# Performance work log

Measured on AMD Instinct MI355X. Metric: run time of the kernel, lower is better.

## Reference

```python
import jax, jax.numpy as jnp
import numpy as np

N = 100000      # nodes
E = 1250000     # edges
D = 64          # d_data
H = 256         # hidden dim
C = 40          # n_cls
K = 4           # propagation steps
ALPHA = 0.05
EPS = 1e-5      # BatchNorm eps


def setup_inputs() -> dict:
    key = jax.random.key(0)
    ks = jax.random.split(key, 8)
    feat = jax.random.normal(ks[0], (N, D), dtype=jnp.float32)
    src = jax.random.randint(ks[1], (E,), 0, N, dtype=jnp.int32)
    dst = jax.random.randint(ks[2], (E,), 0, N, dtype=jnp.int32)
    W1 = jax.random.normal(ks[3], (D, H), dtype=jnp.float32) * (1.0 / np.sqrt(D))
    W2 = jax.random.normal(ks[4], (H, H), dtype=jnp.float32) * (1.0 / np.sqrt(H))
    W3 = jax.random.normal(ks[5], (H, C), dtype=jnp.float32) * (1.0 / np.sqrt(H))
    return {
        "feat": feat, "src": src, "dst": dst,
        "W1": W1, "b1": jnp.zeros((H,), jnp.float32),
        "g1": jnp.ones((H,), jnp.float32), "be1": jnp.zeros((H,), jnp.float32),
        "W2": W2, "b2": jnp.zeros((H,), jnp.float32),
        "g2": jnp.ones((H,), jnp.float32), "be2": jnp.zeros((H,), jnp.float32),
        "W3": W3, "b3": jnp.zeros((C,), jnp.float32),
    }


def _batchnorm(x, gamma, beta):
    # BatchNorm1d in training mode: per-feature batch mean / biased var
    mu = jnp.mean(x, axis=0)
    var = jnp.var(x, axis=0)
    return gamma * (x - mu) * jax.lax.rsqrt(var + EPS) + beta


def reference(feat, src, dst, W1, b1, g1, be1, W2, b2, g2, be2, W3, b3):
    # --- S2GC aggregation: sum_{t=1..K} (D^-1/2 A D^-1/2)^t X ---
    deg = jax.ops.segment_sum(jnp.ones((E,), feat.dtype), dst, num_segments=N)
    norm = jnp.clip(deg, 1.0, None) ** -0.5          # [N]
    norm = norm[:, None]                              # [N,1]
    h = feat
    acc = jnp.zeros_like(feat)
    for _ in range(K):
        h = h * norm
        h = jax.ops.segment_sum(h[src], dst, num_segments=N)  # copy_u -> sum
        h = h * norm
        acc = acc + h
    x = (1.0 - ALPHA) / K * acc + ALPHA * feat
    # --- feat_trans MLP: (Linear -> BN -> ReLU) x2 -> Linear ---
    x = jax.nn.relu(_batchnorm(x @ W1 + b1, g1, be1))
    x = jax.nn.relu(_batchnorm(x @ W2 + b2, g2, be2))
    logits = x @ W3 + b3                              # mask is all-ones (tasks=None)
    return logits
```

## Files before the change

### kernel.cpp

```cpp
#include <hip/hip_runtime.h>

#define NN 100000
#define EE 1250000
#define DD 64
#define HH 256
#define NC_OUT 40
#define ALPHA_C 0.05f
#define COEF 0.2375f
#define EPS_C 1e-5f
#define NBUCK 391
#define EPB 8192
#define GB1 1563
#define NRED 16

typedef __attribute__((ext_vector_type(8))) short short8;
typedef __attribute__((ext_vector_type(4))) float f32x4;

static __device__ __forceinline__ float bf2f(unsigned int u) {
  union { float f; unsigned int i; } x; x.i = u << 16; return x.f;
}
static __device__ __forceinline__ unsigned short f2bf(float f) {
  unsigned int x = __float_as_uint(f);
  unsigned int r = (x + 0x7FFFu + ((x >> 16) & 1u)) >> 16;
  return (unsigned short)r;
}


__global__ void k_count(const int* __restrict__ dst, int* __restrict__ deg) {
  int e = blockIdx.x * 256 + threadIdx.x;
  if (e < EE) atomicAdd(&deg[dst[e]], 1);
}

__global__ void k_scan1(const int* __restrict__ deg, int* __restrict__ rp,
                        int* __restrict__ bsum) {
  __shared__ int ts[256];
  int t = threadIdx.x;
  int base = blockIdx.x * 2048 + t * 8;
  int v[8]; int s = 0;
#pragma unroll
  for (int l = 0; l < 8; l++) { int i = base + l; v[l] = (i < NN) ? deg[i] : 0; s += v[l]; }
  ts[t] = s; __syncthreads();
  for (int off = 1; off < 256; off <<= 1) {
    int x = (t >= off) ? ts[t - off] : 0;
    __syncthreads();
    ts[t] += x;
    __syncthreads();
  }
  int run = ts[t] - s;
#pragma unroll
  for (int l = 0; l < 8; l++) { int i = base + l; if (i < NN) rp[i] = run; run += v[l]; }
  if (t == 255) bsum[blockIdx.x] = ts[255];
}

__global__ void k_scan2(const int* __restrict__ bsum, int* __restrict__ boff, int nb) {
  __shared__ int ts[64];
  int t = threadIdx.x;
  int x = (t < nb) ? bsum[t] : 0;
  ts[t] = x; __syncthreads();
  for (int off = 1; off < 64; off <<= 1) {
    int y = (t >= off) ? ts[t - off] : 0;
    __syncthreads();
    ts[t] += y;
    __syncthreads();
  }
  boff[t] = ts[t] - x;
}

__global__ void k_scan3(int* __restrict__ rp, const int* __restrict__ boff,
                        const int* __restrict__ deg, float* __restrict__ norm,
                        int* __restrict__ bcur) {
  int i = blockIdx.x * 256 + threadIdx.x;
  if (i < NN) {
    int r = rp[i] + boff[i >> 11];
    rp[i] = r;
    if ((i & 255) == 0) bcur[i >> 8] = r;
    int d = deg[i]; if (d < 1) d = 1;
    norm[i] = rsqrtf((float)d);
    if (i == 0) rp[NN] = EE;
  }
}

__global__ __launch_bounds__(256) void k_bucket(const int* __restrict__ src,
                                                const int* __restrict__ dst,
                                                int* __restrict__ bcur,
                                                unsigned int* __restrict__ pairbuf) {
  __shared__ int hist[NBUCK];
  __shared__ int gbase[NBUCK];
  __shared__ int lcur[NBUCK];
  int tid = threadIdx.x;
  int e0 = blockIdx.x * EPB;
  int e1 = e0 + EPB; if (e1 > EE) e1 = EE;
  for (int i = tid; i < NBUCK; i += 256) { hist[i] = 0; lcur[i] = 0; }
  __syncthreads();
  for (int e = e0 + tid; e < e1; e += 256) {
    int b = dst[e] >> 8;
    atomicAdd(&hist[b], 1);
  }
  __syncthreads();
  for (int b = tid; b < NBUCK; b += 256) {
    int h = hist[b];
    gbase[b] = h ? atomicAdd(&bcur[b], h) : 0;
  }
  __syncthreads();
  for (int e = e0 + tid; e < e1; e += 256) {
    int d = dst[e];
    int b = d >> 8;
    int r = atomicAdd(&lcur[b], 1);
    pairbuf[gbase[b] + r] = (unsigned int)src[e] | ((unsigned int)(d & 255) << 24);
  }
}

__global__ __launch_bounds__(256) void k_local(const unsigned int* __restrict__ pairbuf,
                                               const int* __restrict__ rp,
                                               int* __restrict__ srt) {
  __shared__ int cur[256];
  int b = blockIdx.x;
  int node0 = b << 8;
  int t = threadIdx.x;
  int node = node0 + t;
  cur[t] = (node < NN) ? rp[node] : 0;
  int lo = rp[node0];
  int hi = (node0 + 256 <= NN) ? rp[node0 + 256] : EE;
  __syncthreads();
  for (int e = lo + t; e < hi; e += 256) {
    unsigned int w = pairbuf[e];
    int s = (int)(w & 0x1FFFFu);
    int l = (int)(w >> 24);
    int p = atomicAdd(&cur[l], 1);
    srt[p] = s;
  }
}


__global__ void k_init(const float4* __restrict__ feat4, const float* __restrict__ norm,
                       uint2* __restrict__ hs, float4* __restrict__ acc4) {
  int i = blockIdx.x * 256 + threadIdx.x;
  if (i < NN * 16) {
    float nv = norm[i >> 4];
    float4 f = feat4[i];
    uint2 o;
    o.x = (unsigned int)f2bf(f.x * nv) | ((unsigned int)f2bf(f.y * nv) << 16);
    o.y = (unsigned int)f2bf(f.z * nv) | ((unsigned int)f2bf(f.w * nv) << 16);
    hs[i] = o;
    acc4[i] = make_float4(0.f, 0.f, 0.f, 0.f);
  }
}

__global__ void k_gather(const unsigned short* __restrict__ hin,
                         unsigned short* __restrict__ hout,
                         float* __restrict__ accum, const int* __restrict__ rp,
                         const int* __restrict__ srt, const float* __restrict__ norm) {
  int node = blockIdx.x * 4 + (threadIdx.x >> 6);
  int lane = threadIdx.x & 63;
  if (node >= NN) return;
  int beg = rp[node], end = rp[node + 1];
  float s0 = 0.f, s1 = 0.f;
  int e = beg;
  for (; e + 8 <= end; e += 8) {
    int n0 = srt[e], n1 = srt[e + 1], n2 = srt[e + 2], n3 = srt[e + 3];
    int n4 = srt[e + 4], n5 = srt[e + 5], n6 = srt[e + 6], n7 = srt[e + 7];
    float x0 = bf2f(hin[(size_t)n0 * 64 + lane]);
    float x1 = bf2f(hin[(size_t)n1 * 64 + lane]);
    float x2 = bf2f(hin[(size_t)n2 * 64 + lane]);
    float x3 = bf2f(hin[(size_t)n3 * 64 + lane]);
    float x4 = bf2f(hin[(size_t)n4 * 64 + lane]);
    float x5 = bf2f(hin[(size_t)n5 * 64 + lane]);
    float x6 = bf2f(hin[(size_t)n6 * 64 + lane]);
    float x7 = bf2f(hin[(size_t)n7 * 64 + lane]);
    s0 += (x0 + x1) + (x2 + x3);
    s1 += (x4 + x5) + (x6 + x7);
  }
  if (e + 4 <= end) {
    int n0 = srt[e], n1 = srt[e + 1], n2 = srt[e + 2], n3 = srt[e + 3];
    float x0 = bf2f(hin[(size_t)n0 * 64 + lane]);
    float x1 = bf2f(hin[(size_t)n1 * 64 + lane]);
    float x2 = bf2f(hin[(size_t)n2 * 64 + lane]);
    float x3 = bf2f(hin[(size_t)n3 * 64 + lane]);
    s0 += (x0 + x1);
    s1 += (x2 + x3);
    e += 4;
  }
  if (e + 2 <= end) {
    int n0 = srt[e], n1 = srt[e + 1];
    s0 += bf2f(hin[(size_t)n0 * 64 + lane]);
    s1 += bf2f(hin[(size_t)n1 * 64 + lane]);
    e += 2;
  }
  if (e < end) s0 += bf2f(hin[(size_t)srt[e] * 64 + lane]);
  float nv = norm[node];
  float h = (s0 + s1) * nv;
  size_t o = (size_t)node * 64 + lane;
  accum[o] += h;
  hout[o] = f2bf(h * nv);
}

__global__ void k_transW(const float* __restrict__ W, unsigned short* __restrict__ WT, int K) {
  int c = blockIdx.x;
  for (int k = threadIdx.x; k < K; k += blockDim.x)
    WT[(size_t)c * K + k] = f2bf(W[(size_t)k * 256 + c]);
}

template <int KTOT, int MODE>
__global__ __launch_bounds__(256) void k_mfma(
    const void* __restrict__ A0, const float* __restrict__ A1,
    const float* __restrict__ af, const float* __restrict__ cf,
    const unsigned short* __restrict__ BT,
    unsigned short* __restrict__ Yout,
    float* __restrict__ part, int M) {
  constexpr int LDA = 40;
  __shared__ unsigned short Al[64 * LDA];
  __shared__ float afl[256], cfl[256];
  const int tid = threadIdx.x;
  const int wid = tid >> 6, lane = tid & 63;
  const int rbase = blockIdx.x * 64;
  const int nbase = wid * 64;
  const int lr = lane & 15;
  const int kg = lane >> 4;

  if constexpr (MODE == 1) {
    afl[tid] = af[tid];
    cfl[tid] = cf[tid];
    __syncthreads();
  }

  f32x4 acc[4][4];
#pragma unroll
  for (int i = 0; i < 4; i++)
#pragma unroll
    for (int j = 0; j < 4; j++) acc[i][j] = (f32x4){0.f, 0.f, 0.f, 0.f};

  for (int k0 = 0; k0 < KTOT; k0 += 32) {
    {
      int r = tid >> 2;
      int c8 = (tid & 3) * 8;
      int row = rbase + r; if (row >= M) row = M - 1;
      float xv[8];
      if constexpr (MODE == 0) {
        const float* ap = (const float*)A0 + (size_t)row * 64 + k0 + c8;
        const float* fp = A1 + (size_t)row * 64 + k0 + c8;
        float4 a0 = *(const float4*)ap, a1v = *(const float4*)(ap + 4);
        float4 f0 = *(const float4*)fp, f1 = *(const float4*)(fp + 4);
        xv[0] = COEF * a0.x + ALPHA_C * f0.x; xv[1] = COEF * a0.y + ALPHA_C * f0.y;
        xv[2] = COEF * a0.z + ALPHA_C * f0.z; xv[3] = COEF * a0.w + ALPHA_C * f0.w;
        xv[4] = COEF * a1v.x + ALPHA_C * f1.x; xv[5] = COEF * a1v.y + ALPHA_C * f1.y;
        xv[6] = COEF * a1v.z + ALPHA_C * f1.z; xv[7] = COEF * a1v.w + ALPHA_C * f1.w;
      } else {
        const unsigned short* Yp = (const unsigned short*)A0 + (size_t)row * 256 + k0 + c8;
        uint4 v = *(const uint4*)Yp;
        unsigned int u[4] = { v.x, v.y, v.z, v.w };
#pragma unroll
        for (int h = 0; h < 4; h++) {
          int kc = k0 + c8 + h * 2;
          xv[h * 2]     = fmaxf(fmaf(afl[kc],     bf2f(u[h] & 0xffffu), cfl[kc]),     0.f);
          xv[h * 2 + 1] = fmaxf(fmaf(afl[kc + 1], bf2f(u[h] >> 16),     cfl[kc + 1]), 0.f);
        }
      }
      uint4 pk;
      pk.x = (unsigned int)f2bf(xv[0]) | ((unsigned int)f2bf(xv[1]) << 16);
      pk.y = (unsigned int)f2bf(xv[2]) | ((unsigned int)f2bf(xv[3]) << 16);
      pk.z = (unsigned int)f2bf(xv[4]) | ((unsigned int)f2bf(xv[5]) << 16);
      pk.w = (unsigned int)f2bf(xv[6]) | ((unsigned int)f2bf(xv[7]) << 16);
      *(uint4*)&Al[r * LDA + c8] = pk;
    }
    __syncthreads();

    short8 bfrag[4];
#pragma unroll
    for (int ni = 0; ni < 4; ni++) {
      int col = nbase + ni * 16 + lr;
      bfrag[ni] = *(const short8*)(BT + (size_t)col * KTOT + k0 + kg * 8);
    }
    short8 afrag[4];
#pragma unroll
    for (int mi = 0; mi < 4; mi++) {
      afrag[mi] = *(const short8*)&Al[(mi * 16 + lr) * LDA + kg * 8];
    }
#pragma unroll
    for (int mi = 0; mi < 4; mi++)
#pragma unroll
      for (int ni = 0; ni < 4; ni++)
        acc[mi][ni] = __builtin_amdgcn_mfma_f32_16x16x32_bf16(afrag[mi], bfrag[ni],
                                                              acc[mi][ni], 0, 0, 0);
    __syncthreads();
  }

#pragma unroll
  for (int mi = 0; mi < 4; mi++) {
#pragma unroll
    for (int reg = 0; reg < 4; reg++) {
      int row = rbase + mi * 16 + kg * 4 + reg;
      if (row < M) {
#pragma unroll
        for (int ni = 0; ni < 4; ni++) {
          int col = nbase + ni * 16 + lr;
          Yout[(size_t)row * 256 + col] = f2bf(acc[mi][ni][reg]);
        }
      }
    }
  }

  float s4[4] = {0.f, 0.f, 0.f, 0.f};
  float q4[4] = {0.f, 0.f, 0.f, 0.f};
#pragma unroll
  for (int mi = 0; mi < 4; mi++) {
#pragma unroll
    for (int reg = 0; reg < 4; reg++) {
      int row = rbase + mi * 16 + kg * 4 + reg;
      if (row < M) {
#pragma unroll
        for (int ni = 0; ni < 4; ni++) {
          float v = acc[mi][ni][reg];
          s4[ni] += v;
          q4[ni] = fmaf(v, v, q4[ni]);
        }
      }
    }
  }
  float* pb = part + (size_t)blockIdx.x * 512;
#pragma unroll
  for (int ni = 0; ni < 4; ni++) {
    float s = s4[ni], q = q4[ni];
    s += __shfl_xor(s, 16); s += __shfl_xor(s, 32);
    q += __shfl_xor(q, 16); q += __shfl_xor(q, 32);
    if (kg == 0) {
      int col = nbase + ni * 16 + lr;
      pb[col] = s;
      pb[256 + col] = q;
    }
  }
}

__global__ __launch_bounds__(512) void k_red(const float* __restrict__ part,
                                             float* __restrict__ red2) {
  int t = threadIdx.x;
  const int per = (GB1 + NRED - 1) / NRED;
  int b0 = blockIdx.x * per;
  int b1 = b0 + per; if (b1 > GB1) b1 = GB1;
  float s = 0.f;
  for (int b = b0; b < b1; b++) s += part[(size_t)b * 512 + t];
  red2[(size_t)blockIdx.x * 512 + t] = s;
}

__global__ void k_fold(const float* __restrict__ red2,
                       const float* __restrict__ gam, const float* __restrict__ bet,
                       float* __restrict__ af, float* __restrict__ cfv) {
  int c = threadIdx.x;
  float s = 0.f, q = 0.f;
#pragma unroll
  for (int r = 0; r < NRED; r++) {
    s += red2[(size_t)r * 512 + c];
    q += red2[(size_t)r * 512 + 256 + c];
  }
  float m = s * (1.0f / NN);
  float var = q * (1.0f / NN) - m * m;
  float a = gam[c] * rsqrtf(var + EPS_C);
  af[c] = a;
  cfv[c] = bet[c] - m * a;
}

__global__ __launch_bounds__(256) void k_gemm3(
    const unsigned short* __restrict__ Y2, const float* __restrict__ af,
    const float* __restrict__ cfv, const float* __restrict__ W3,
    const float* __restrict__ b3, float* __restrict__ out, int M) {
  __shared__ float Al[256 * 33];
  __shared__ float Wl[256 * 40];
  __shared__ float afl[256], cfl[256];
  int tid = threadIdx.x;
#pragma unroll
  for (int l = 0; l < 40; l++) Wl[l * 256 + tid] = W3[l * 256 + tid];
  afl[tid] = af[tid]; cfl[tid] = cfv[tid];
  __syncthreads();
  int rbase = blockIdx.x * 256;
  int rg = tid >> 3;
  int cg = tid & 7;
  float acc[8][5];
#pragma unroll
  for (int i = 0; i < 8; i++)
#pragma unroll
    for (int j = 0; j < 5; j++) acc[i][j] = 0.f;

  for (int k0 = 0; k0 < 256; k0 += 32) {
    int row = rbase + tid; if (row >= M) row = M - 1;
    const uint4* p = (const uint4*)(Y2 + (size_t)row * 256 + k0);
    uint4 vv[4]; vv[0] = p[0]; vv[1] = p[1]; vv[2] = p[2]; vv[3] = p[3];
    float* ap = &Al[tid * 33];
#pragma unroll
    for (int q = 0; q < 4; q++) {
      unsigned int u[4] = { vv[q].x, vv[q].y, vv[q].z, vv[q].w };
#pragma unroll
      for (int h = 0; h < 4; h++) {
        int kc = k0 + q * 8 + h * 2;
        float x0 = bf2f(u[h] & 0xffffu);
        float x1 = bf2f(u[h] >> 16);
        x0 = fmaxf(fmaf(afl[kc], x0, cfl[kc]), 0.f);
        x1 = fmaxf(fmaf(afl[kc + 1], x1, cfl[kc + 1]), 0.f);
        ap[q * 8 + h * 2] = x0; ap[q * 8 + h * 2 + 1] = x1;
      }
    }
    __syncthreads();
#pragma unroll 4
    for (int kk = 0; kk < 32; kk++) {
      float b[5];
#pragma unroll
      for (int j = 0; j < 5; j++) b[j] = Wl[(k0 + kk) * 40 + cg * 5 + j];
#pragma unroll
      for (int i = 0; i < 8; i++) {
        float a = Al[(rg + 32 * i) * 33 + kk];
#pragma unroll
        for (int j = 0; j < 5; j++) acc[i][j] = fmaf(a, b[j], acc[i][j]);
      }
    }
    __syncthreads();
  }
#pragma unroll
  for (int i = 0; i < 8; i++) {
    int row = rbase + rg + 32 * i;
    if (row < M) {
#pragma unroll
      for (int j = 0; j < 5; j++)
        out[(size_t)row * 40 + cg * 5 + j] = acc[i][j] + b3[cg * 5 + j];
    }
  }
}


extern "C" void kernel_launch(void* const* d_in, const int* in_sizes, int n_in,
                              void* d_out, int out_size, void* d_ws, size_t ws_size,
                              hipStream_t stream) {
  const float* feat = (const float*)d_in[0];
  const int* src = (const int*)d_in[1];
  const int* dstv = (const int*)d_in[2];
  const float* W1 = (const float*)d_in[3];
  const float* g1 = (const float*)d_in[5];
  const float* be1 = (const float*)d_in[6];
  const float* W2 = (const float*)d_in[7];
  const float* g2 = (const float*)d_in[9];
  const float* be2 = (const float*)d_in[10];
  const float* W3 = (const float*)d_in[11];
  const float* b3 = (const float*)d_in[12];
  float* out = (float*)d_out;

  char* w = (char*)d_ws;
  size_t off = 0;
  auto alloc = [&](size_t bytes) -> char* {
    char* p = w + off;
    off = (off + bytes + 255) & ~(size_t)255;
    return p;
  };
  int* deg = (int*)alloc((size_t)NN * 4);
  int* rp = (int*)alloc((size_t)(NN + 1) * 4);
  int* bsum = (int*)alloc(256);
  int* boff = (int*)alloc(256);
  int* bcur = (int*)alloc((size_t)NBUCK * 4);
  float* norm = (float*)alloc((size_t)NN * 4);
  int* srt = (int*)alloc((size_t)EE * 4);
  unsigned int* pairbuf = (unsigned int*)alloc((size_t)EE * 4);
  unsigned short* hsA = (unsigned short*)alloc((size_t)NN * 64 * 2);
  unsigned short* hsB = (unsigned short*)alloc((size_t)NN * 64 * 2);
  float* accb = (float*)alloc((size_t)NN * 64 * 4);
  unsigned short* Y1 = (unsigned short*)alloc((size_t)NN * 256 * 2);
  unsigned short* Y2 = (unsigned short*)alloc((size_t)NN * 256 * 2);
  unsigned short* W1T = (unsigned short*)alloc(256 * 64 * 2);
  unsigned short* W2T = (unsigned short*)alloc(256 * 256 * 2);
  float* part = (float*)alloc((size_t)GB1 * 512 * 4);
  float* red2 = (float*)alloc((size_t)NRED * 512 * 4);
  float* a1 = (float*)alloc(256 * 4);
  float* c1 = (float*)alloc(256 * 4);
  float* a2 = (float*)alloc(256 * 4);
  float* c2 = (float*)alloc(256 * 4);

  hipMemsetAsync(deg, 0, (size_t)NN * 4, stream);

  const int EB = (EE + 255) / 256;
  const int NB = (NN + 255) / 256;
  const int SB = (NN + 2047) / 2048;
  const int BB = (EE + EPB - 1) / EPB;

  k_count<<<EB, 256, 0, stream>>>(dstv, deg);
  k_transW<<<256, 64, 0, stream>>>(W1, W1T, 64);
  k_transW<<<256, 256, 0, stream>>>(W2, W2T, 256);
  k_scan1<<<SB, 256, 0, stream>>>(deg, rp, bsum);
  k_scan2<<<1, 64, 0, stream>>>(bsum, boff, SB);
  k_scan3<<<NB, 256, 0, stream>>>(rp, boff, deg, norm, bcur);
  k_bucket<<<BB, 256, 0, stream>>>(src, dstv, bcur, pairbuf);
  k_local<<<NBUCK, 256, 0, stream>>>(pairbuf, rp, srt);

  k_init<<<(NN * 16 + 255) / 256, 256, 0, stream>>>((const float4*)feat, norm,
                                                    (uint2*)hsA, (float4*)accb);
  k_gather<<<(NN + 3) / 4, 256, 0, stream>>>(hsA, hsB, accb, rp, srt, norm);
  k_gather<<<(NN + 3) / 4, 256, 0, stream>>>(hsB, hsA, accb, rp, srt, norm);
  k_gather<<<(NN + 3) / 4, 256, 0, stream>>>(hsA, hsB, accb, rp, srt, norm);
  k_gather<<<(NN + 3) / 4, 256, 0, stream>>>(hsB, hsA, accb, rp, srt, norm);

  k_mfma<64, 0><<<GB1, 256, 0, stream>>>(accb, feat, nullptr, nullptr, W1T, Y1, part, NN);
  k_red<<<NRED, 512, 0, stream>>>(part, red2);
  k_fold<<<1, 256, 0, stream>>>(red2, g1, be1, a1, c1);
  k_mfma<256, 1><<<GB1, 256, 0, stream>>>(Y1, nullptr, a1, c1, W2T, Y2, part, NN);
  k_red<<<NRED, 512, 0, stream>>>(part, red2);
  k_fold<<<1, 256, 0, stream>>>(red2, g2, be2, a2, c2);
  k_gemm3<<<NB, 256, 0, stream>>>(Y2, a2, c2, W3, b3, out, NN);
}
```

Baseline: 577.7 us.

## Double-buffer MFMA A tiles, stage output via LDS, prefetch gather indices

The GEMM kernel now double-buffers the A tile in shared memory and loads the next K-slices into registers ahead of use, which removes one barrier per K step and overlaps global loads with MFMA. The output tile is packed to bf16 pairs, staged through a swizzled LDS buffer and written back with coalesced 16-byte stores instead of scattered 2-byte stores. The gather kernel software-prefetches the next 8 neighbor indices before issuing the current feature loads. In exchange the kernel uses more shared memory (32 KB) and more registers, which may reduce occupancy.

```diff
diff --git a/kernel.cpp b/kernel.cpp
--- a/kernel.cpp
+++ b/kernel.cpp
@@ -156,19 +156,31 @@
   int beg = rp[node], end = rp[node + 1];
   float s0 = 0.f, s1 = 0.f;
   int e = beg;
-  for (; e + 8 <= end; e += 8) {
-    int n0 = srt[e], n1 = srt[e + 1], n2 = srt[e + 2], n3 = srt[e + 3];
-    int n4 = srt[e + 4], n5 = srt[e + 5], n6 = srt[e + 6], n7 = srt[e + 7];
-    float x0 = bf2f(hin[(size_t)n0 * 64 + lane]);
-    float x1 = bf2f(hin[(size_t)n1 * 64 + lane]);
-    float x2 = bf2f(hin[(size_t)n2 * 64 + lane]);
-    float x3 = bf2f(hin[(size_t)n3 * 64 + lane]);
-    float x4 = bf2f(hin[(size_t)n4 * 64 + lane]);
-    float x5 = bf2f(hin[(size_t)n5 * 64 + lane]);
-    float x6 = bf2f(hin[(size_t)n6 * 64 + lane]);
-    float x7 = bf2f(hin[(size_t)n7 * 64 + lane]);
-    s0 += (x0 + x1) + (x2 + x3);
-    s1 += (x4 + x5) + (x6 + x7);
+  if (e + 8 <= end) {
+    int i0 = srt[e],     i1 = srt[e + 1], i2 = srt[e + 2], i3 = srt[e + 3];
+    int i4 = srt[e + 4], i5 = srt[e + 5], i6 = srt[e + 6], i7 = srt[e + 7];
+    while (true) {
+      int ne = e + 8;
+      bool more = (ne + 8 <= end);
+      int j0, j1, j2, j3, j4, j5, j6, j7;
+      if (more) {
+        j0 = srt[ne];     j1 = srt[ne + 1]; j2 = srt[ne + 2]; j3 = srt[ne + 3];
+        j4 = srt[ne + 4]; j5 = srt[ne + 5]; j6 = srt[ne + 6]; j7 = srt[ne + 7];
+      }
+      float x0 = bf2f(hin[(size_t)i0 * 64 + lane]);
+      float x1 = bf2f(hin[(size_t)i1 * 64 + lane]);
+      float x2 = bf2f(hin[(size_t)i2 * 64 + lane]);
+      float x3 = bf2f(hin[(size_t)i3 * 64 + lane]);
+      float x4 = bf2f(hin[(size_t)i4 * 64 + lane]);
+      float x5 = bf2f(hin[(size_t)i5 * 64 + lane]);
+      float x6 = bf2f(hin[(size_t)i6 * 64 + lane]);
+      float x7 = bf2f(hin[(size_t)i7 * 64 + lane]);
+      s0 += (x0 + x1) + (x2 + x3);
+      s1 += (x4 + x5) + (x6 + x7);
+      e = ne;
+      if (!more) break;
+      i0 = j0; i1 = j1; i2 = j2; i3 = j3; i4 = j4; i5 = j5; i6 = j6; i7 = j7;
+    }
   }
   if (e + 4 <= end) {
     int n0 = srt[e], n1 = srt[e + 1], n2 = srt[e + 2], n3 = srt[e + 3];
@@ -207,15 +219,23 @@
     const unsigned short* __restrict__ BT,
     unsigned short* __restrict__ Yout,
     float* __restrict__ part, int M) {
+  constexpr int S = KTOT / 32;
   constexpr int LDA = 40;
-  __shared__ unsigned short Al[64 * LDA];
+  __shared__ __align__(16) unsigned char smemraw[32768];
+  unsigned short* const Al0 = (unsigned short*)smemraw;
+  unsigned short* const Al1 = (unsigned short*)(smemraw + 5120);
+  unsigned int* const Cl = (unsigned int*)smemraw;
   __shared__ float afl[256], cfl[256];
+
   const int tid = threadIdx.x;
   const int wid = tid >> 6, lane = tid & 63;
   const int rbase = blockIdx.x * 64;
   const int nbase = wid * 64;
   const int lr = lane & 15;
   const int kg = lane >> 4;
+  const int r = tid >> 2;
+  const int c8 = (tid & 3) * 8;
+  int arow = rbase + r; if (arow >= M) arow = M - 1;
 
   if constexpr (MODE == 1) {
     afl[tid] = af[tid];
@@ -223,81 +243,86 @@
     __syncthreads();
   }
 
+  uint4 rw[2];
+
+  auto LOADX = [&](int s, int buf) {
+    float xv[8];
+    if constexpr (MODE == 0) {
+      const float* ap = (const float*)A0 + (size_t)arow * 64 + s * 32 + c8;
+      const float* fp = A1 + (size_t)arow * 64 + s * 32 + c8;
+      float4 a0 = *(const float4*)ap, a1v = *(const float4*)(ap + 4);
+      float4 f0 = *(const float4*)fp, f1 = *(const float4*)(fp + 4);
+      xv[0] = COEF * a0.x + ALPHA_C * f0.x;  xv[1] = COEF * a0.y + ALPHA_C * f0.y;
+      xv[2] = COEF * a0.z + ALPHA_C * f0.z;  xv[3] = COEF * a0.w + ALPHA_C * f0.w;
+      xv[4] = COEF * a1v.x + ALPHA_C * f1.x; xv[5] = COEF * a1v.y + ALPHA_C * f1.y;
+      xv[6] = COEF * a1v.z + ALPHA_C * f1.z; xv[7] = COEF * a1v.w + ALPHA_C * f1.w;
+    } else {
+      uint4 v = *(const uint4*)((const unsigned short*)A0 + (size_t)arow * 256 + s * 32 + c8);
+      unsigned int u[4] = { v.x, v.y, v.z, v.w };
+#pragma unroll
+      for (int h = 0; h < 4; h++) {
+        int kc = s * 32 + c8 + h * 2;
+        xv[h * 2]     = fmaxf(fmaf(afl[kc],     bf2f(u[h] & 0xffffu), cfl[kc]),     0.f);
+        xv[h * 2 + 1] = fmaxf(fmaf(afl[kc + 1], bf2f(u[h] >> 16),     cfl[kc + 1]), 0.f);
+      }
+    }
+    uint4 pk;
+    pk.x = (unsigned int)f2bf(xv[0]) | ((unsigned int)f2bf(xv[1]) << 16);
+    pk.y = (unsigned int)f2bf(xv[2]) | ((unsigned int)f2bf(xv[3]) << 16);
+    pk.z = (unsigned int)f2bf(xv[4]) | ((unsigned int)f2bf(xv[5]) << 16);
+    pk.w = (unsigned int)f2bf(xv[6]) | ((unsigned int)f2bf(xv[7]) << 16);
+    rw[buf] = pk;
+  };
+
   f32x4 acc[4][4];
 #pragma unroll
   for (int i = 0; i < 4; i++)
 #pragma unroll
     for (int j = 0; j < 4; j++) acc[i][j] = (f32x4){0.f, 0.f, 0.f, 0.f};
 
-  for (int k0 = 0; k0 < KTOT; k0 += 32) {
-    {
-      int r = tid >> 2;
-      int c8 = (tid & 3) * 8;
-      int row = rbase + r; if (row >= M) row = M - 1;
-      float xv[8];
-      if constexpr (MODE == 0) {
-        const float* ap = (const float*)A0 + (size_t)row * 64 + k0 + c8;
-        const float* fp = A1 + (size_t)row * 64 + k0 + c8;
-        float4 a0 = *(const float4*)ap, a1v = *(const float4*)(ap + 4);
-        float4 f0 = *(const float4*)fp, f1 = *(const float4*)(fp + 4);
-        xv[0] = COEF * a0.x + ALPHA_C * f0.x; xv[1] = COEF * a0.y + ALPHA_C * f0.y;
-        xv[2] = COEF * a0.z + ALPHA_C * f0.z; xv[3] = COEF * a0.w + ALPHA_C * f0.w;
-        xv[4] = COEF * a1v.x + ALPHA_C * f1.x; xv[5] = COEF * a1v.y + ALPHA_C * f1.y;
-        xv[6] = COEF * a1v.z + ALPHA_C * f1.z; xv[7] = COEF * a1v.w + ALPHA_C * f1.w;
-      } else {
-        const unsigned short* Yp = (const unsigned short*)A0 + (size_t)row * 256 + k0 + c8;
-        uint4 v = *(const uint4*)Yp;
-        unsigned int u[4] = { v.x, v.y, v.z, v.w };
-#pragma unroll
-        for (int h = 0; h < 4; h++) {
-          int kc = k0 + c8 + h * 2;
-          xv[h * 2]     = fmaxf(fmaf(afl[kc],     bf2f(u[h] & 0xffffu), cfl[kc]),     0.f);
-          xv[h * 2 + 1] = fmaxf(fmaf(afl[kc + 1], bf2f(u[h] >> 16),     cfl[kc + 1]), 0.f);
-        }
-      }
-      uint4 pk;
-      pk.x = (unsigned int)f2bf(xv[0]) | ((unsigned int)f2bf(xv[1]) << 16);
-      pk.y = (unsigned int)f2bf(xv[2]) | ((unsigned int)f2bf(xv[3]) << 16);
-      pk.z = (unsigned int)f2bf(xv[4]) | ((unsigned int)f2bf(xv[5]) << 16);
-      pk.w = (unsigned int)f2bf(xv[6]) | ((unsigned int)f2bf(xv[7]) << 16);
-      *(uint4*)&Al[r * LDA + c8] = pk;
-    }
-    __syncthreads();
-
+  LOADX(0, 0);
+  if constexpr (S > 1) LOADX(1, 1);
+  *(uint4*)&Al0[r * LDA + c8] = rw[0];
+
+#pragma unroll
+  for (int s = 0; s < S; s++) {
+    __syncthreads();
+    const unsigned short* Alr = (s & 1) ? Al1 : Al0;
+    unsigned short* Alw = (s & 1) ? Al0 : Al1;
     short8 bfrag[4];
 #pragma unroll
-    for (int ni = 0; ni < 4; ni++) {
-      int col = nbase + ni * 16 + lr;
-      bfrag[ni] = *(const short8*)(BT + (size_t)col * KTOT + k0 + kg * 8);
-    }
+    for (int ni = 0; ni < 4; ni++)
+      bfrag[ni] = *(const short8*)(BT + (size_t)(nbase + ni * 16 + lr) * KTOT + s * 32 + kg * 8);
+    if (s + 1 < S) *(uint4*)&Alw[r * LDA + c8] = rw[(s + 1) & 1];
+    if (s + 2 < S) LOADX(s + 2, s & 1);
     short8 afrag[4];
 #pragma unroll
-    for (int mi = 0; mi < 4; mi++) {
-      afrag[mi] = *(const short8*)&Al[(mi * 16 + lr) * LDA + kg * 8];
-    }
+    for (int mi = 0; mi < 4; mi++)
+      afrag[mi] = *(const short8*)&Alr[(mi * 16 + lr) * LDA + kg * 8];
 #pragma unroll
     for (int mi = 0; mi < 4; mi++)
 #pragma unroll
       for (int ni = 0; ni < 4; ni++)
         acc[mi][ni] = __builtin_amdgcn_mfma_f32_16x16x32_bf16(afrag[mi], bfrag[ni],
                                                               acc[mi][ni], 0, 0, 0);
-    __syncthreads();
-  }
-
-#pragma unroll
-  for (int mi = 0; mi < 4; mi++) {
-#pragma unroll
-    for (int reg = 0; reg < 4; reg++) {
-      int row = rbase + mi * 16 + kg * 4 + reg;
-      if (row < M) {
-#pragma unroll
-        for (int ni = 0; ni < 4; ni++) {
-          int col = nbase + ni * 16 + lr;
-          Yout[(size_t)row * 256 + col] = f2bf(acc[mi][ni][reg]);
+  }
+
+  __syncthreads();
+#pragma unroll
+  for (int mi = 0; mi < 4; mi++)
+#pragma unroll
+    for (int ni = 0; ni < 4; ni++)
+#pragma unroll
+      for (int reg = 0; reg < 4; reg++) {
+        float v = acc[mi][ni][reg];
+        float pv = __shfl_xor(v, 1);
+        if (!(lr & 1)) {
+          int row = mi * 16 + kg * 4 + reg;
+          int cd = (nbase >> 1) + ni * 8 + (lr >> 1);
+          unsigned int pk = (unsigned int)f2bf(v) | ((unsigned int)f2bf(pv) << 16);
+          Cl[row * 128 + (cd ^ (kg << 3))] = pk;
         }
       }
-    }
-  }
 
   float s4[4] = {0.f, 0.f, 0.f, 0.f};
   float q4[4] = {0.f, 0.f, 0.f, 0.f};
@@ -327,6 +352,19 @@
       pb[col] = s;
       pb[256 + col] = q;
     }
+  }
+
+  __syncthreads();
+#pragma unroll
+  for (int p = 0; p < 8; p++) {
+    int flat = p * 256 + tid;
+    int row = flat >> 5;
+    int u4 = flat & 31;
+    int m = ((row >> 2) & 3) << 3;
+    uint4 vv = *(const uint4*)&Cl[row * 128 + ((u4 * 4) ^ m)];
+    int grow = rbase + row;
+    if (grow < M)
+      *(uint4*)(Yout + (size_t)grow * 256 + u4 * 8) = vv;
   }
 }
 
```

New measurement: 603.7 us. 4.5% more time.

## Drop fp32 accumulator; keep per-step bf16 hops and sum them in GEMM1

Applied to the files above, without the earlier changes.

The gather kernels no longer read-modify-write a float32 accumulator each step. Each propagation step now writes its own bf16 buffer holding h*norm^2, and the first MFMA GEMM sums the four buffers and rescales by sqrt(deg)*COEF while loading the A tile. This removes about 25 MB of fp32 accumulator traffic per step and the zeroing in k_init, at the cost of extra buffers and bf16 rounding on every stored hop. Separately, the MFMA kernels move to 512-thread blocks with 128-row tiles, and weights are pre-laid out per 32-wide K slice so B fragment loads are contiguous.

```diff
diff --git a/kernel.cpp b/kernel.cpp
--- a/kernel.cpp
+++ b/kernel.cpp
@@ -10,7 +10,8 @@
 #define EPS_C 1e-5f
 #define NBUCK 391
 #define EPB 8192
-#define GB1 1563
+#define NB2 782
+#define PART_ROWS (NB2 * 2)
 #define NRED 16
 
 typedef __attribute__((ext_vector_type(8))) short short8;
@@ -23,6 +24,10 @@
   unsigned int x = __float_as_uint(f);
   unsigned int r = (x + 0x7FFFu + ((x >> 16) & 1u)) >> 16;
   return (unsigned short)r;
+}
+static __device__ __forceinline__ float bfat(uint4 v, int j) {
+  unsigned int u = ((const unsigned int*)&v)[j >> 1];
+  return bf2f((j & 1) ? (u >> 16) : (u & 0xffffu));
 }
 
 
@@ -68,7 +73,7 @@
 
 __global__ void k_scan3(int* __restrict__ rp, const int* __restrict__ boff,
                         const int* __restrict__ deg, float* __restrict__ norm,
-                        int* __restrict__ bcur) {
+                        float* __restrict__ rnorm, int* __restrict__ bcur) {
   int i = blockIdx.x * 256 + threadIdx.x;
   if (i < NN) {
     int r = rp[i] + boff[i >> 11];
@@ -76,6 +81,7 @@
     if ((i & 255) == 0) bcur[i >> 8] = r;
     int d = deg[i]; if (d < 1) d = 1;
     norm[i] = rsqrtf((float)d);
+    rnorm[i] = sqrtf((float)d);
     if (i == 0) rp[NN] = EE;
   }
 }
@@ -133,7 +139,7 @@
 
 
 __global__ void k_init(const float4* __restrict__ feat4, const float* __restrict__ norm,
-                       uint2* __restrict__ hs, float4* __restrict__ acc4) {
+                       uint2* __restrict__ hs) {
   int i = blockIdx.x * 256 + threadIdx.x;
   if (i < NN * 16) {
     float nv = norm[i >> 4];
@@ -142,13 +148,12 @@
     o.x = (unsigned int)f2bf(f.x * nv) | ((unsigned int)f2bf(f.y * nv) << 16);
     o.y = (unsigned int)f2bf(f.z * nv) | ((unsigned int)f2bf(f.w * nv) << 16);
     hs[i] = o;
-    acc4[i] = make_float4(0.f, 0.f, 0.f, 0.f);
   }
 }
 
 __global__ void k_gather(const unsigned short* __restrict__ hin,
                          unsigned short* __restrict__ hout,
-                         float* __restrict__ accum, const int* __restrict__ rp,
+                         const int* __restrict__ rp,
                          const int* __restrict__ srt, const float* __restrict__ norm) {
   int node = blockIdx.x * 4 + (threadIdx.x >> 6);
   int lane = threadIdx.x & 63;
@@ -188,38 +193,46 @@
   }
   if (e < end) s0 += bf2f(hin[(size_t)srt[e] * 64 + lane]);
   float nv = norm[node];
-  float h = (s0 + s1) * nv;
-  size_t o = (size_t)node * 64 + lane;
-  accum[o] += h;
-  hout[o] = f2bf(h * nv);
-}
-
-__global__ void k_transW(const float* __restrict__ W, unsigned short* __restrict__ WT, int K) {
-  int c = blockIdx.x;
-  for (int k = threadIdx.x; k < K; k += blockDim.x)
-    WT[(size_t)c * K + k] = f2bf(W[(size_t)k * 256 + c]);
+  hout[(size_t)node * 64 + lane] = f2bf((s0 + s1) * nv * nv);
+}
+
+__global__ void k_transWT(const float* __restrict__ W, unsigned short* __restrict__ BTt,
+                          int K) {
+  int col = blockIdx.x;
+  int t = threadIdx.x;
+  if (t >= (K >> 3)) return;
+  int s = t >> 2, kg = t & 3;
+  size_t o = (size_t)s * 8192 + (size_t)col * 32 + kg * 8;
+#pragma unroll
+  for (int j = 0; j < 8; j++)
+    BTt[o + j] = f2bf(W[(size_t)(s * 32 + kg * 8 + j) * 256 + col]);
 }
 
 template <int KTOT, int MODE>
-__global__ __launch_bounds__(256) void k_mfma(
-    const void* __restrict__ A0, const float* __restrict__ A1,
+__global__ __launch_bounds__(512) void k_mfma(
+    const unsigned short* __restrict__ h1, const unsigned short* __restrict__ h2,
+    const unsigned short* __restrict__ h3, const unsigned short* __restrict__ h4,
+    const float* __restrict__ feat, const float* __restrict__ rnorm,
+    const unsigned short* __restrict__ Yin,
     const float* __restrict__ af, const float* __restrict__ cf,
-    const unsigned short* __restrict__ BT,
-    unsigned short* __restrict__ Yout,
-    float* __restrict__ part, int M) {
+    const unsigned short* __restrict__ BTt,
+    unsigned short* __restrict__ Yout, float* __restrict__ part, int M) {
+  constexpr int S = KTOT / 32;
   constexpr int LDA = 40;
-  __shared__ unsigned short Al[64 * LDA];
+  __shared__ unsigned short Al[128 * LDA];
   __shared__ float afl[256], cfl[256];
   const int tid = threadIdx.x;
   const int wid = tid >> 6, lane = tid & 63;
-  const int rbase = blockIdx.x * 64;
-  const int nbase = wid * 64;
+  const int rowg = wid >> 2, colg = wid & 3;
+  const int rbase = blockIdx.x * 128;
   const int lr = lane & 15;
   const int kg = lane >> 4;
+  const int r = tid >> 2;
+  const int c8 = (tid & 3) * 8;
+  int arow = rbase + r; if (arow >= M) arow = M - 1;
 
   if constexpr (MODE == 1) {
-    afl[tid] = af[tid];
-    cfl[tid] = cf[tid];
+    if (tid < 256) { afl[tid] = af[tid]; cfl[tid] = cf[tid]; }
     __syncthreads();
   }
 
@@ -229,28 +242,30 @@
 #pragma unroll
     for (int j = 0; j < 4; j++) acc[i][j] = (f32x4){0.f, 0.f, 0.f, 0.f};
 
-  for (int k0 = 0; k0 < KTOT; k0 += 32) {
+  for (int s = 0; s < S; s++) {
     {
-      int r = tid >> 2;
-      int c8 = (tid & 3) * 8;
-      int row = rbase + r; if (row >= M) row = M - 1;
       float xv[8];
       if constexpr (MODE == 0) {
-        const float* ap = (const float*)A0 + (size_t)row * 64 + k0 + c8;
-        const float* fp = A1 + (size_t)row * 64 + k0 + c8;
-        float4 a0 = *(const float4*)ap, a1v = *(const float4*)(ap + 4);
+        size_t ho = (size_t)arow * 64 + s * 32 + c8;
+        uint4 v1 = *(const uint4*)(h1 + ho);
+        uint4 v2 = *(const uint4*)(h2 + ho);
+        uint4 v3 = *(const uint4*)(h3 + ho);
+        uint4 v4 = *(const uint4*)(h4 + ho);
+        float rc = rnorm[arow] * COEF;
+        const float* fp = feat + ho;
         float4 f0 = *(const float4*)fp, f1 = *(const float4*)(fp + 4);
-        xv[0] = COEF * a0.x + ALPHA_C * f0.x; xv[1] = COEF * a0.y + ALPHA_C * f0.y;
-        xv[2] = COEF * a0.z + ALPHA_C * f0.z; xv[3] = COEF * a0.w + ALPHA_C * f0.w;
-        xv[4] = COEF * a1v.x + ALPHA_C * f1.x; xv[5] = COEF * a1v.y + ALPHA_C * f1.y;
-        xv[6] = COEF * a1v.z + ALPHA_C * f1.z; xv[7] = COEF * a1v.w + ALPHA_C * f1.w;
+        float ff[8] = { f0.x, f0.y, f0.z, f0.w, f1.x, f1.y, f1.z, f1.w };
+#pragma unroll
+        for (int j = 0; j < 8; j++) {
+          float sm = (bfat(v1, j) + bfat(v2, j)) + (bfat(v3, j) + bfat(v4, j));
+          xv[j] = rc * sm + ALPHA_C * ff[j];
+        }
       } else {
-        const unsigned short* Yp = (const unsigned short*)A0 + (size_t)row * 256 + k0 + c8;
-        uint4 v = *(const uint4*)Yp;
+        uint4 v = *(const uint4*)(Yin + (size_t)arow * 256 + s * 32 + c8);
         unsigned int u[4] = { v.x, v.y, v.z, v.w };
 #pragma unroll
         for (int h = 0; h < 4; h++) {
-          int kc = k0 + c8 + h * 2;
+          int kc = s * 32 + c8 + h * 2;
           xv[h * 2]     = fmaxf(fmaf(afl[kc],     bf2f(u[h] & 0xffffu), cfl[kc]),     0.f);
           xv[h * 2 + 1] = fmaxf(fmaf(afl[kc + 1], bf2f(u[h] >> 16),     cfl[kc + 1]), 0.f);
         }
@@ -267,14 +282,13 @@
     short8 bfrag[4];
 #pragma unroll
     for (int ni = 0; ni < 4; ni++) {
-      int col = nbase + ni * 16 + lr;
-      bfrag[ni] = *(const short8*)(BT + (size_t)col * KTOT + k0 + kg * 8);
+      int col = colg * 64 + ni * 16 + lr;
+      bfrag[ni] = *(const short8*)(BTt + (size_t)s * 8192 + (size_t)col * 32 + kg * 8);
     }
     short8 afrag[4];
 #pragma unroll
-    for (int mi = 0; mi < 4; mi++) {
-      afrag[mi] = *(const short8*)&Al[(mi * 16 + lr) * LDA + kg * 8];
-    }
+    for (int mi = 0; mi < 4; mi++)
+      afrag[mi] = *(const short8*)&Al[(rowg * 64 + mi * 16 + lr) * LDA + kg * 8];
 #pragma unroll
     for (int mi = 0; mi < 4; mi++)
 #pragma unroll
@@ -288,11 +302,11 @@
   for (int mi = 0; mi < 4; mi++) {
 #pragma unroll
     for (int reg = 0; reg < 4; reg++) {
-      int row = rbase + mi * 16 + kg * 4 + reg;
+      int row = rbase + rowg * 64 + mi * 16 + kg * 4 + reg;
       if (row < M) {
 #pragma unroll
         for (int ni = 0; ni < 4; ni++) {
-          int col = nbase + ni * 16 + lr;
+          int col = colg * 64 + ni * 16 + lr;
           Yout[(size_t)row * 256 + col] = f2bf(acc[mi][ni][reg]);
         }
       }
@@ -305,7 +319,7 @@
   for (int mi = 0; mi < 4; mi++) {
 #pragma unroll
     for (int reg = 0; reg < 4; reg++) {
-      int row = rbase + mi * 16 + kg * 4 + reg;
+      int row = rbase + rowg * 64 + mi * 16 + kg * 4 + reg;
       if (row < M) {
 #pragma unroll
         for (int ni = 0; ni < 4; ni++) {
@@ -316,14 +330,14 @@
       }
     }
   }
-  float* pb = part + (size_t)blockIdx.x * 512;
+  float* pb = part + ((size_t)blockIdx.x * 2 + rowg) * 512;
 #pragma unroll
   for (int ni = 0; ni < 4; ni++) {
     float s = s4[ni], q = q4[ni];
     s += __shfl_xor(s, 16); s += __shfl_xor(s, 32);
     q += __shfl_xor(q, 16); q += __shfl_xor(q, 32);
     if (kg == 0) {
-      int col = nbase + ni * 16 + lr;
+      int col = colg * 64 + ni * 16 + lr;
       pb[col] = s;
       pb[256 + col] = q;
     }
@@ -333,9 +347,9 @@
 __global__ __launch_bounds__(512) void k_red(const float* __restrict__ part,
                                              float* __restrict__ red2) {
   int t = threadIdx.x;
-  const int per = (GB1 + NRED - 1) / NRED;
+  const int per = (PART_ROWS + NRED - 1) / NRED;
   int b0 = blockIdx.x * per;
-  int b1 = b0 + per; if (b1 > GB1) b1 = GB1;
+  int b1 = b0 + per; if (b1 > PART_ROWS) b1 = PART_ROWS;
   float s = 0.f;
   for (int b = b0; b < b1; b++) s += part[(size_t)b * 512 + t];
   red2[(size_t)blockIdx.x * 512 + t] = s;
@@ -453,16 +467,19 @@
   int* boff = (int*)alloc(256);
   int* bcur = (int*)alloc((size_t)NBUCK * 4);
   float* norm = (float*)alloc((size_t)NN * 4);
+  float* rnorm = (float*)alloc((size_t)NN * 4);
   int* srt = (int*)alloc((size_t)EE * 4);
   unsigned int* pairbuf = (unsigned int*)alloc((size_t)EE * 4);
-  unsigned short* hsA = (unsigned short*)alloc((size_t)NN * 64 * 2);
-  unsigned short* hsB = (unsigned short*)alloc((size_t)NN * 64 * 2);
-  float* accb = (float*)alloc((size_t)NN * 64 * 4);
+  unsigned short* hs0 = (unsigned short*)alloc((size_t)NN * 64 * 2);
+  unsigned short* hn1 = (unsigned short*)alloc((size_t)NN * 64 * 2);
+  unsigned short* hn2 = (unsigned short*)alloc((size_t)NN * 64 * 2);
+  unsigned short* hn3 = (unsigned short*)alloc((size_t)NN * 64 * 2);
+  unsigned short* hn4 = (unsigned short*)alloc((size_t)NN * 64 * 2);
   unsigned short* Y1 = (unsigned short*)alloc((size_t)NN * 256 * 2);
   unsigned short* Y2 = (unsigned short*)alloc((size_t)NN * 256 * 2);
   unsigned short* W1T = (unsigned short*)alloc(256 * 64 * 2);
   unsigned short* W2T = (unsigned short*)alloc(256 * 256 * 2);
-  float* part = (float*)alloc((size_t)GB1 * 512 * 4);
+  float* part = (float*)alloc((size_t)PART_ROWS * 512 * 4);
   float* red2 = (float*)alloc((size_t)NRED * 512 * 4);
   float* a1 = (float*)alloc(256 * 4);
   float* c1 = (float*)alloc(256 * 4);
@@ -477,25 +494,26 @@
   const int BB = (EE + EPB - 1) / EPB;
 
   k_count<<<EB, 256, 0, stream>>>(dstv, deg);
-  k_transW<<<256, 64, 0, stream>>>(W1, W1T, 64);
-  k_transW<<<256, 256, 0, stream>>>(W2, W2T, 256);
+  k_transWT<<<256, 64, 0, stream>>>(W1, W1T, 64);
+  k_transWT<<<256, 64, 0, stream>>>(W2, W2T, 256);
   k_scan1<<<SB, 256, 0, stream>>>(deg, rp, bsum);
   k_scan2<<<1, 64, 0, stream>>>(bsum, boff, SB);
-  k_scan3<<<NB, 256, 0, stream>>>(rp, boff, deg, norm, bcur);
+  k_scan3<<<NB, 256, 0, stream>>>(rp, boff, deg, norm, rnorm, bcur);
   k_bucket<<<BB, 256, 0, stream>>>(src, dstv, bcur, pairbuf);
   k_local<<<NBUCK, 256, 0, stream>>>(pairbuf, rp, srt);
 
-  k_init<<<(NN * 16 + 255) / 256, 256, 0, stream>>>((const float4*)feat, norm,
-                                                    (uint2*)hsA, (float4*)accb);
-  k_gather<<<(NN + 3) / 4, 256, 0, stream>>>(hsA, hsB, accb, rp, srt, norm);
-  k_gather<<<(NN + 3) / 4, 256, 0, stream>>>(hsB, hsA, accb, rp, srt, norm);
-  k_gather<<<(NN + 3) / 4, 256, 0, stream>>>(hsA, hsB, accb, rp, srt, norm);
-  k_gather<<<(NN + 3) / 4, 256, 0, stream>>>(hsB, hsA, accb, rp, srt, norm);
-
-  k_mfma<64, 0><<<GB1, 256, 0, stream>>>(accb, feat, nullptr, nullptr, W1T, Y1, part, NN);
+  k_init<<<(NN * 16 + 255) / 256, 256, 0, stream>>>((const float4*)feat, norm, (uint2*)hs0);
+  k_gather<<<(NN + 3) / 4, 256, 0, stream>>>(hs0, hn1, rp, srt, norm);
+  k_gather<<<(NN + 3) / 4, 256, 0, stream>>>(hn1, hn2, rp, srt, norm);
+  k_gather<<<(NN + 3) / 4, 256, 0, stream>>>(hn2, hn3, rp, srt, norm);
+  k_gather<<<(NN + 3) / 4, 256, 0, stream>>>(hn3, hn4, rp, srt, norm);
+
+  k_mfma<64, 0><<<NB2, 512, 0, stream>>>(hn1, hn2, hn3, hn4, feat, rnorm,
+                                         nullptr, nullptr, nullptr, W1T, Y1, part, NN);
   k_red<<<NRED, 512, 0, stream>>>(part, red2);
   k_fold<<<1, 256, 0, stream>>>(red2, g1, be1, a1, c1);
-  k_mfma<256, 1><<<GB1, 256, 0, stream>>>(Y1, nullptr, a1, c1, W2T, Y2, part, NN);
+  k_mfma<256, 1><<<NB2, 512, 0, stream>>>(nullptr, nullptr, nullptr, nullptr, nullptr,
+                                          nullptr, Y1, a1, c1, W2T, Y2, part, NN);
   k_red<<<NRED, 512, 0, stream>>>(part, red2);
   k_fold<<<1, 256, 0, stream>>>(red2, g2, be2, a2, c2);
   k_gemm3<<<NB, 256, 0, stream>>>(Y2, a2, c2, W3, b3, out, NN);
```

Result: faster. 562.1 us (-2.7%).
